# Optimization experiments

Hardware: AMD Instinct MI355X
Metric: run time of the kernel (lower is better)

Reference implementation:

```python
import jax, jax.numpy as jnp
import numpy as np

N = 50000
E = 800000
HEADS = 4
C = 64  # per-head channels
IN = 256
NEG_SLOPE = 0.2


def setup_inputs() -> dict:
    key = jax.random.key(0)
    k = jax.random.split(key, 6)
    x = jax.random.normal(k[0], (N, IN), dtype=jnp.float32)
    edge_index = jax.random.randint(k[1], (2, E), 0, N, dtype=jnp.int64)
    # Glorot-ish scale for weights
    W = jax.random.normal(k[2], (IN, HEADS * C), dtype=jnp.float32) * (1.0 / np.sqrt(IN))
    att_src = jax.random.normal(k[3], (HEADS, C), dtype=jnp.float32) * (1.0 / np.sqrt(C))
    att_dst = jax.random.normal(k[4], (HEADS, C), dtype=jnp.float32) * (1.0 / np.sqrt(C))
    bias = jax.random.normal(k[5], (HEADS * C,), dtype=jnp.float32) * 0.02
    return {"x": x, "edge_index": edge_index, "W": W, "att_src": att_src,
            "att_dst": att_dst, "bias": bias}


def _gat_forward(x, edge_index, W, att_src, att_dst, bias):
    n = x.shape[0]
    h = (x @ W).reshape(n, HEADS, C)  # [N, H, C]

    # add self loops (PyG default add_self_loops=True)
    loop = jnp.arange(n, dtype=edge_index.dtype)
    src = jnp.concatenate([edge_index[0], loop])  # [E+N]
    dst = jnp.concatenate([edge_index[1], loop])

    # per-node attention contributions  [N, H]
    a_src = jnp.einsum('nhc,hc->nh', h, att_src)
    a_dst = jnp.einsum('nhc,hc->nh', h, att_dst)

    # edge logits with leaky relu  [E+N, H]
    logits = a_src[src] + a_dst[dst]
    logits = jnp.where(logits >= 0, logits, NEG_SLOPE * logits)

    # segment softmax over destination neighborhoods
    seg_max = jax.ops.segment_max(logits, dst, num_segments=n)  # [N, H]
    seg_max = jnp.where(jnp.isfinite(seg_max), seg_max, 0.0)
    ex = jnp.exp(logits - seg_max[dst])
    denom = jax.ops.segment_sum(ex, dst, num_segments=n)  # [N, H]
    alpha = ex / (denom[dst] + 1e-16)  # [E+N, H]

    # weighted scatter-add of source messages
    msgs = alpha[:, :, None] * h[src]  # [E+N, H, C]
    out = jax.ops.segment_sum(msgs, dst, num_segments=n)  # [N, H, C]
    out = out.reshape(n, HEADS * C) + bias
    return jax.nn.relu(out)


def reference(x, edge_index, W, att_src, att_dst, bias):
    return _gat_forward(x, edge_index, W, att_src, att_dst, bias)
```

## Files before the change

### kernel.cpp

```cpp
#include <hip/hip_runtime.h>
#include <hip/hip_bf16.h>
#include <math.h>

#define NEG 0.2f
#define BSH 5
#define EPB 2048

typedef __attribute__((ext_vector_type(4))) float f4;
typedef __attribute__((ext_vector_type(8))) short s8;
typedef __attribute__((ext_vector_type(2))) __fp16 h2;

__device__ __forceinline__ short f2bf(float f) {
    unsigned u = __float_as_uint(f);
    u += 0x7fff + ((u >> 16) & 1);
    return (short)(u >> 16);
}
__device__ __forceinline__ unsigned pk2(float a, float b) {
    union { __hip_bfloat162 h; unsigned u; } c;
    c.h = __float22bfloat162_rn(make_float2(a, b));
    return c.u;
}
__device__ __forceinline__ unsigned pkh(float a, float b) {
    union { h2 h; unsigned u; } c;
    c.h = __builtin_amdgcn_cvt_pkrtz(a, b);
    return c.u;
}
__device__ __forceinline__ void fma8(float* acc, float w, uint4 v) {
    union { uint4 u; __fp16 h[8]; } c; c.u = v;
#pragma unroll
    for (int k = 0; k < 8; ++k) acc[k] = fmaf(w, (float)c.h[k], acc[k]);
}

__global__ __launch_bounds__(256) void prep_count(
    const float* __restrict__ W, short* __restrict__ Wt, int* __restrict__ off,
    const int* __restrict__ ei, int* __restrict__ hist2d,
    int E, int N, int NBUCK, int NB, int Etot)
{
    const int blk = blockIdx.x, t = threadIdx.x;
    if (blk < 256) {
        int id = blk * 256 + t;
        int n = id >> 8, k = id & 255;
        Wt[id] = f2bf(W[k * 256 + n]);
        if (id == 0) off[N] = Etot;
        return;
    }
    extern __shared__ int lh[];
    const int cblk = blk - 256;
    for (int b = t; b < NBUCK; b += 256) lh[b] = 0;
    __syncthreads();
    const int e0 = cblk * EPB;
    if (e0 + EPB <= E) {
#pragma unroll
        for (int i = 0; i < EPB / 1024; ++i) {
            int e = e0 + i * 1024 + t * 4;
            int4 d = *(const int4*)(ei + E + e);
            atomicAdd(&lh[d.x >> BSH], 1);
            atomicAdd(&lh[d.y >> BSH], 1);
            atomicAdd(&lh[d.z >> BSH], 1);
            atomicAdd(&lh[d.w >> BSH], 1);
        }
    } else {
        for (int i = 0; i < EPB / 256; ++i) {
            int e = e0 + i * 256 + t;
            if (e < Etot) {
                int dte = (e < E) ? ei[E + e] : (e - E);
                atomicAdd(&lh[dte >> BSH], 1);
            }
        }
    }
    __syncthreads();
    for (int b = t; b < NBUCK; b += 256) hist2d[b * NB + cblk] = lh[b];
}

__global__ __launch_bounds__(512) void gemm_attn(
    const float* __restrict__ x, const short* __restrict__ Wt,
    const float* __restrict__ att_src, const float* __restrict__ att_dst,
    short* __restrict__ hb, float* __restrict__ a_src_n,
    float* __restrict__ a_dst_n, int M)
{
    __shared__ __align__(16) short xs[2][128][32];
    const int t = threadIdx.x;
    const int lane = t & 63, wv = t >> 6;
    const int wr = wv >> 2;
    const int hd = wv & 3;
    const int quad = lane >> 4, l15 = lane & 15;
    const int n0 = blockIdx.x * 128;

    const int row = t >> 2, kq = t & 3;
    const bool okr = (n0 + row) < M;
    const float* xp = x + (size_t)(n0 + row) * 256 + kq * 8;

    const short* wbase = Wt + (size_t)(hd * 64 + l15) * 256 + quad * 8;

    f4 acc[4][4];
#pragma unroll
    for (int i = 0; i < 4; ++i)
#pragma unroll
        for (int j = 0; j < 4; ++j) acc[i][j] = (f4)(0.f);

    float4 v0 = {}, v1 = {};
    if (okr) { const float4* p = (const float4*)xp; v0 = p[0]; v1 = p[1]; }

    int buf = 0;
#pragma unroll
    for (int ks = 0; ks < 8; ++ks) {
        uint4 u = { pk2(v0.x, v0.y), pk2(v0.z, v0.w), pk2(v1.x, v1.y), pk2(v1.z, v1.w) };
        *(uint4*)&xs[buf][row][kq * 8] = u;
        __syncthreads();

        if (ks < 7 && okr) {
            const float4* p = (const float4*)(xp + (ks + 1) * 32);
            v0 = p[0]; v1 = p[1];
        }

        s8 af[4], bf[4];
#pragma unroll
        for (int i = 0; i < 4; ++i)
            af[i] = *(const s8*)(wbase + (size_t)(i * 16) * 256 + ks * 32);
#pragma unroll
        for (int j = 0; j < 4; ++j)
            bf[j] = *(const s8*)&xs[buf][wr * 64 + j * 16 + l15][quad * 8];
#pragma unroll
        for (int i = 0; i < 4; ++i)
#pragma unroll
            for (int j = 0; j < 4; ++j)
                acc[i][j] = __builtin_amdgcn_mfma_f32_16x16x32_bf16(af[i], bf[j], acc[i][j], 0, 0, 0);
        buf ^= 1;
    }

    float asv[4][4], adv[4][4];
#pragma unroll
    for (int i = 0; i < 4; ++i)
#pragma unroll
        for (int rr = 0; rr < 4; ++rr) {
            asv[i][rr] = att_src[hd * 64 + i * 16 + quad * 4 + rr];
            adv[i][rr] = att_dst[hd * 64 + i * 16 + quad * 4 + rr];
        }

#pragma unroll
    for (int j = 0; j < 4; ++j) {
        const int node = n0 + wr * 64 + j * 16 + l15;
        const bool ok = node < M;
        float ps = 0.f, pd = 0.f;
#pragma unroll
        for (int i = 0; i < 4; ++i)
#pragma unroll
            for (int rr = 0; rr < 4; ++rr) {
                float v = acc[i][j][rr];
                ps = fmaf(v, asv[i][rr], ps);
                pd = fmaf(v, adv[i][rr], pd);
            }
        ps += __shfl_xor(ps, 16); ps += __shfl_xor(ps, 32);
        pd += __shfl_xor(pd, 16); pd += __shfl_xor(pd, 32);
        if (ok && quad == 0) {
            a_src_n[node * 4 + hd] = ps;
            a_dst_n[node * 4 + hd] = pd;
        }
        if (ok) {
#pragma unroll
            for (int i = 0; i < 4; ++i) {
                uint2 pk = make_uint2(pkh(acc[i][j][0], acc[i][j][1]),
                                      pkh(acc[i][j][2], acc[i][j][3]));
                *(uint2*)&hb[(size_t)node * 256 + hd * 64 + i * 16 + quad * 4] = pk;
            }
        }
    }
}

__global__ __launch_bounds__(1024) void scan1(const int* __restrict__ src,
                                              int* __restrict__ dst,
                                              int* __restrict__ bsum, int Ntot)
{
    __shared__ int wsum[16], wexc[16];
    const int t = threadIdx.x, lane = t & 63, w = t >> 6;
    const int idx = blockIdx.x * 1024 + t;
    int v = (idx < Ntot) ? src[idx] : 0;
    int val = v;
#pragma unroll
    for (int o = 1; o < 64; o <<= 1) {
        int u = __shfl_up(val, o);
        if (lane >= o) val += u;
    }
    if (lane == 63) wsum[w] = val;
    __syncthreads();
    if (t < 16) {
        int s = wsum[t];
#pragma unroll
        for (int o = 1; o < 16; o <<= 1) {
            int u = __shfl_up(s, o, 16);
            if (t >= o) s += u;
        }
        wexc[t] = s - wsum[t];
        if (t == 15) bsum[blockIdx.x] = s;
    }
    __syncthreads();
    if (idx < Ntot) dst[idx] = wexc[w] + val - v;
}

__global__ __launch_bounds__(1024) void scan2v(const int* __restrict__ bsum,
                                               int* __restrict__ bexc, int nb)
{
    __shared__ int wsum[16], wexc[16];
    const int t = threadIdx.x, lane = t & 63, w = t >> 6;
    int v = (t < nb) ? bsum[t] : 0;
    int val = v;
#pragma unroll
    for (int o = 1; o < 64; o <<= 1) {
        int u = __shfl_up(val, o);
        if (lane >= o) val += u;
    }
    if (lane == 63) wsum[w] = val;
    __syncthreads();
    if (t < 16) {
        int s = wsum[t];
#pragma unroll
        for (int o = 1; o < 16; o <<= 1) {
            int u = __shfl_up(s, o, 16);
            if (t >= o) s += u;
        }
        wexc[t] = s - wsum[t];
    }
    __syncthreads();
    if (t < nb) bexc[t] = wexc[w] + val - v;
}

__global__ __launch_bounds__(256) void scatter2(const int* __restrict__ ei,
                                                const int* __restrict__ scanned,
                                                const int* __restrict__ bexc,
                                                unsigned* __restrict__ bucketed,
                                                int E, int N, int NBUCK, int NB)
{
    extern __shared__ int lcur[];
    const int t = threadIdx.x, blk = blockIdx.x;
    for (int b = t; b < NBUCK; b += 256) {
        int idx = b * NB + blk;
        lcur[b] = scanned[idx] + bexc[idx >> 10];
    }
    __syncthreads();
    const int e0 = blk * EPB, Etot = E + N;
    if (e0 + EPB <= E) {
#pragma unroll
        for (int i = 0; i < EPB / 1024; ++i) {
            int e = e0 + i * 1024 + t * 4;
            int4 s4 = *(const int4*)(ei + e);
            int4 d4 = *(const int4*)(ei + E + e);
            int p0 = atomicAdd(&lcur[d4.x >> BSH], 1);
            bucketed[p0] = (unsigned)s4.x | ((unsigned)(d4.x & 31) << 20);
            int p1 = atomicAdd(&lcur[d4.y >> BSH], 1);
            bucketed[p1] = (unsigned)s4.y | ((unsigned)(d4.y & 31) << 20);
            int p2 = atomicAdd(&lcur[d4.z >> BSH], 1);
            bucketed[p2] = (unsigned)s4.z | ((unsigned)(d4.z & 31) << 20);
            int p3 = atomicAdd(&lcur[d4.w >> BSH], 1);
            bucketed[p3] = (unsigned)s4.w | ((unsigned)(d4.w & 31) << 20);
        }
    } else {
        for (int i = 0; i < EPB / 256; ++i) {
            int e = e0 + i * 256 + t;
            if (e < Etot) {
                int src, dte;
                if (e < E) { src = ei[e]; dte = ei[E + e]; }
                else       { src = e - E; dte = src; }
                int pos = atomicAdd(&lcur[dte >> BSH], 1);
                bucketed[pos] = (unsigned)src | ((unsigned)(dte & 31) << 20);
            }
        }
    }
}

__global__ __launch_bounds__(256) void csr_build(
    const unsigned* __restrict__ bucketed, const int* __restrict__ scanned,
    const int* __restrict__ bexc, int* __restrict__ off, int* __restrict__ csr,
    int N, int NB, int NBUCK, int Etot)
{
    __shared__ unsigned est[2048];
    __shared__ int ldeg4[4][32], lcur4[4][32], loff[32];
    const int t = threadIdx.x, wv = t >> 6, b = blockIdx.x;

    const int i0 = b * NB;
    const int gbase = scanned[i0] + bexc[i0 >> 10];
    int gend;
    if (b + 1 == NBUCK) gend = Etot;
    else { int i1 = (b + 1) * NB; gend = scanned[i1] + bexc[i1 >> 10]; }
    int cnt = gend - gbase;
    if (cnt > 2048) cnt = 2048;

    if (t < 128) ldeg4[t >> 5][t & 31] = 0;
    __syncthreads();
    for (int i = t; i < cnt; i += 256) {
        unsigned en = bucketed[gbase + i];
        est[i] = en;
        atomicAdd(&ldeg4[wv][en >> 20], 1);
    }
    __syncthreads();
    if (t < 32) {
        int d0 = ldeg4[0][t], d1 = ldeg4[1][t], d2 = ldeg4[2][t], d3 = ldeg4[3][t];
        int tot = d0 + d1 + d2 + d3;
        int val = tot;
#pragma unroll
        for (int o = 1; o < 32; o <<= 1) {
            int u = __shfl_up(val, o, 32);
            if (t >= o) val += u;
        }
        int excl = val - tot;
        loff[t] = excl;
        lcur4[0][t] = excl;
        lcur4[1][t] = excl + d0;
        lcur4[2][t] = excl + d0 + d1;
        lcur4[3][t] = excl + d0 + d1 + d2;
    }
    __syncthreads();
    for (int i = t; i < cnt; i += 256) {
        unsigned en = est[i];
        int pos = atomicAdd(&lcur4[wv][en >> 20], 1);
        csr[gbase + pos] = (int)(en & 0xFFFFF);
    }
    if (t < 32) {
        int n = (b << BSH) + t;
        if (n < N) off[n] = gbase + loff[t];
    }
}

__global__ __launch_bounds__(256) void aggregate(const short* __restrict__ hb,
                                                 const float* __restrict__ a_src_n,
                                                 const float* __restrict__ a_dst_n,
                                                 const int* __restrict__ off,
                                                 const int* __restrict__ csr,
                                                 const float* __restrict__ bias,
                                                 float* __restrict__ out, int N)
{
    __shared__ float lds_w[4][64][4];
    __shared__ int   lds_s[4][64];
    const int wv = threadIdx.x >> 6;
    const int lane = threadIdx.x & 63;
    const int half = lane >> 5, l31 = lane & 31;
    const int n = blockIdx.x * 4 + wv;
    if (n >= N) return;

    const int base = off[n];
    const int d = off[n + 1] - base;
    const float4 ad = *(const float4*)(a_dst_n + 4 * n);
    const int hl = l31 >> 3;

    float acc[8] = {0.f, 0.f, 0.f, 0.f, 0.f, 0.f, 0.f, 0.f};
    float4 sum = make_float4(0.f, 0.f, 0.f, 0.f);
    const uint4* hp = (const uint4*)hb;

    for (int c0 = 0; c0 < d; c0 += 64) {
        int j = c0 + lane;
        int s = 0;
        float4 w4 = make_float4(0.f, 0.f, 0.f, 0.f);
        if (j < d) {
            s = csr[base + j];
            float4 as = *(const float4*)(a_src_n + 4 * s);
            float lx = as.x + ad.x; lx = lx >= 0.f ? lx : NEG * lx;
            float ly = as.y + ad.y; ly = ly >= 0.f ? ly : NEG * ly;
            float lz = as.z + ad.z; lz = lz >= 0.f ? lz : NEG * lz;
            float lw = as.w + ad.w; lw = lw >= 0.f ? lw : NEG * lw;
            w4 = make_float4(__expf(lx), __expf(ly), __expf(lz), __expf(lw));
        }
        sum.x += w4.x; sum.y += w4.y; sum.z += w4.z; sum.w += w4.w;
        *(float4*)&lds_w[wv][lane][0] = w4;
        lds_s[wv][lane] = s;
        __builtin_amdgcn_wave_barrier();

        const int cl = (d - c0) < 64 ? (d - c0) : 64;
        int jj = 0;
        for (; jj + 8 <= cl; jj += 8) {
            int   s0 = lds_s[wv][jj + half];
            int   s1 = lds_s[wv][jj + 2 + half];
            int   s2 = lds_s[wv][jj + 4 + half];
            int   s3 = lds_s[wv][jj + 6 + half];
            float w0 = lds_w[wv][jj + half][hl];
            float w1 = lds_w[wv][jj + 2 + half][hl];
            float w2 = lds_w[wv][jj + 4 + half][hl];
            float w3 = lds_w[wv][jj + 6 + half][hl];
            uint4 v0 = hp[(size_t)s0 * 32 + l31];
            uint4 v1 = hp[(size_t)s1 * 32 + l31];
            uint4 v2 = hp[(size_t)s2 * 32 + l31];
            uint4 v3 = hp[(size_t)s3 * 32 + l31];
            fma8(acc, w0, v0);
            fma8(acc, w1, v1);
            fma8(acc, w2, v2);
            fma8(acc, w3, v3);
        }
        for (; jj < cl; jj += 2) {
            int   s0 = lds_s[wv][jj + half];
            float w0 = lds_w[wv][jj + half][hl];
            uint4 v0 = hp[(size_t)s0 * 32 + l31];
            fma8(acc, w0, v0);
        }
        __builtin_amdgcn_wave_barrier();
    }

#pragma unroll
    for (int k = 0; k < 8; ++k) acc[k] += __shfl_xor(acc[k], 32);

#pragma unroll
    for (int o = 32; o > 0; o >>= 1) {
        sum.x += __shfl_xor(sum.x, o);
        sum.y += __shfl_xor(sum.y, o);
        sum.z += __shfl_xor(sum.z, o);
        sum.w += __shfl_xor(sum.w, o);
    }
    float sh = (hl & 2) ? ((hl & 1) ? sum.w : sum.z) : ((hl & 1) ? sum.y : sum.x);
    float ih = 1.f / (sh + 1e-16f);

    if (half == 0) {
        const float4* bp = (const float4*)bias + l31 * 2;
        float4 b0 = bp[0], b1 = bp[1];
        float4 o0, o1;
        o0.x = fmaxf(fmaf(acc[0], ih, b0.x), 0.f);
        o0.y = fmaxf(fmaf(acc[1], ih, b0.y), 0.f);
        o0.z = fmaxf(fmaf(acc[2], ih, b0.z), 0.f);
        o0.w = fmaxf(fmaf(acc[3], ih, b0.w), 0.f);
        o1.x = fmaxf(fmaf(acc[4], ih, b1.x), 0.f);
        o1.y = fmaxf(fmaf(acc[5], ih, b1.y), 0.f);
        o1.z = fmaxf(fmaf(acc[6], ih, b1.z), 0.f);
        o1.w = fmaxf(fmaf(acc[7], ih, b1.w), 0.f);
        float4* op = (float4*)(out + (size_t)n * 256) + l31 * 2;
        op[0] = o0;
        op[1] = o1;
    }
}

extern "C" void kernel_launch(void* const* d_in, const int* in_sizes, int n_in,
                              void* d_out, int out_size, void* d_ws, size_t ws_size,
                              hipStream_t stream)
{
    const float* x       = (const float*)d_in[0];
    const int*   ei      = (const int*)d_in[1];
    const float* W       = (const float*)d_in[2];
    const float* att_src = (const float*)d_in[3];
    const float* att_dst = (const float*)d_in[4];
    const float* bias    = (const float*)d_in[5];
    float* out = (float*)d_out;

    const int N = in_sizes[0] / 256;
    const int E = in_sizes[1] / 2;
    const int Etot = E + N;
    const int NBUCK = (N + 31) >> BSH;
    const int NB = (Etot + EPB - 1) / EPB;
    const int Ntot = NBUCK * NB;
    const int nb1 = (Ntot + 1023) / 1024;

    char* p = (char*)d_ws;
    short*    hb      = (short*)p;    p += (size_t)N * 256 * sizeof(short);
    short*    Wt      = (short*)p;    p += 256 * 256 * sizeof(short);
    float*    a_src_n = (float*)p;    p += (size_t)N * 4 * sizeof(float);
    float*    a_dst_n = (float*)p;    p += (size_t)N * 4 * sizeof(float);
    int*      hist2d  = (int*)p;      p += (size_t)Ntot * sizeof(int);
    int*      scanned = (int*)p;      p += (size_t)Ntot * sizeof(int);
    int*      bsum    = (int*)p;      p += 1024 * sizeof(int);
    int*      bexc    = (int*)p;      p += 1024 * sizeof(int);
    int*      off     = (int*)p;      p += (size_t)(N + 1) * sizeof(int);
    unsigned* bucketed= (unsigned*)p; p += (size_t)Etot * sizeof(unsigned);
    int*      csr     = (int*)p;      p += (size_t)Etot * sizeof(int);

    prep_count<<<256 + NB, 256, NBUCK * sizeof(int), stream>>>(
        W, Wt, off, ei, hist2d, E, N, NBUCK, NB, Etot);
    gemm_attn<<<(N + 127) / 128, 512, 0, stream>>>(
        x, Wt, att_src, att_dst, hb, a_src_n, a_dst_n, N);
    scan1<<<nb1, 1024, 0, stream>>>(hist2d, scanned, bsum, Ntot);
    scan2v<<<1, 1024, 0, stream>>>(bsum, bexc, nb1);
    scatter2<<<NB, 256, NBUCK * sizeof(int), stream>>>(ei, scanned, bexc, bucketed,
                                                       E, N, NBUCK, NB);
    csr_build<<<NBUCK, 256, 0, stream>>>(bucketed, scanned, bexc, off, csr,
                                         N, NB, NBUCK, Etot);
    aggregate<<<(N + 3) / 4, 256, 0, stream>>>(hb, a_src_n, a_dst_n, off, csr,
                                               bias, out, N);
}
```

Measured before the change: 234.0 us.

## Process two nodes per wave with software-pipelined gather in aggregate

The aggregate kernel now gives each half-wave (32 lanes) its own destination node, so a wave handles two nodes and the grid is halved. Source indices are broadcast with shuffles instead of through LDS. The per-chunk gather is unrolled over 32 edges, keeping eight row loads in flight ahead of the FMAs. This removes the cross-half accumulator reduction and aims to hide gather latency, at the cost of more registers and divergence when the two nodes' degrees differ.

```diff
diff --git a/kernel.cpp b/kernel.cpp
--- a/kernel.cpp
+++ b/kernel.cpp
@@ -329,29 +329,46 @@
                                                  float* __restrict__ out, int N)
 {
     __shared__ float lds_w[4][64][4];
-    __shared__ int   lds_s[4][64];
-    const int wv = threadIdx.x >> 6;
-    const int lane = threadIdx.x & 63;
+    const int t = threadIdx.x, wv = t >> 6, lane = t & 63;
     const int half = lane >> 5, l31 = lane & 31;
-    const int n = blockIdx.x * 4 + wv;
-    if (n >= N) return;
-
-    const int base = off[n];
-    const int d = off[n + 1] - base;
-    const float4 ad = *(const float4*)(a_dst_n + 4 * n);
+    const int hsel = lane & 32;
+    const int n = blockIdx.x * 8 + wv * 2 + half;
+    const bool okn = n < N;
+    const int nc = okn ? n : (N - 1);
+
+    const int base = off[nc];
+    const int d = off[nc + 1] - base;
+    const float4 ad = *(const float4*)(a_dst_n + 4 * nc);
     const int hl = l31 >> 3;
+    const uint4* hp = (const uint4*)hb;
 
     float acc[8] = {0.f, 0.f, 0.f, 0.f, 0.f, 0.f, 0.f, 0.f};
     float4 sum = make_float4(0.f, 0.f, 0.f, 0.f);
-    const uint4* hp = (const uint4*)hb;
-
-    for (int c0 = 0; c0 < d; c0 += 64) {
-        int j = c0 + lane;
-        int s = 0;
+
+    int dm = d; { int o = __shfl_xor(d, 32); dm = dm > o ? dm : o; }
+    const int tc = (dm + 31) >> 5;
+
+    for (int c = 0; c < tc; ++c) {
+        const int c0 = c << 5;
+        const int j = c0 + l31;
+        const int jc = (j < d) ? j : (d - 1);
+        const int s_my = csr[base + jc];
+
+        const int cl = d - c0;
+        const int Sown = cl < 0 ? 0 : (cl > 32 ? 32 : cl);
+        int S = Sown; { int o = __shfl_xor(Sown, 32); S = S > o ? S : o; }
+
+        const float4 as = *(const float4*)(a_src_n + 4 * s_my);
+
+        uint4 va0 = {}, va1 = {}, va2 = {}, va3 = {};
+        uint4 vb0 = {}, vb1 = {}, vb2 = {}, vb3 = {};
+#define ISS(K, V) if ((K) < S) { int sk = __shfl(s_my, hsel | (K)); \
+                                 V = hp[(size_t)sk * 32 + l31]; }
+        ISS(0, va0) ISS(1, va1) ISS(2, va2) ISS(3, va3)
+        ISS(4, vb0) ISS(5, vb1) ISS(6, vb2) ISS(7, vb3)
+
         float4 w4 = make_float4(0.f, 0.f, 0.f, 0.f);
         if (j < d) {
-            s = csr[base + j];
-            float4 as = *(const float4*)(a_src_n + 4 * s);
             float lx = as.x + ad.x; lx = lx >= 0.f ? lx : NEG * lx;
             float ly = as.y + ad.y; ly = ly >= 0.f ? ly : NEG * ly;
             float lz = as.z + ad.z; lz = lz >= 0.f ? lz : NEG * lz;
@@ -360,43 +377,27 @@
         }
         sum.x += w4.x; sum.y += w4.y; sum.z += w4.z; sum.w += w4.w;
         *(float4*)&lds_w[wv][lane][0] = w4;
-        lds_s[wv][lane] = s;
         __builtin_amdgcn_wave_barrier();
 
-        const int cl = (d - c0) < 64 ? (d - c0) : 64;
-        int jj = 0;
-        for (; jj + 8 <= cl; jj += 8) {
-            int   s0 = lds_s[wv][jj + half];
-            int   s1 = lds_s[wv][jj + 2 + half];
-            int   s2 = lds_s[wv][jj + 4 + half];
-            int   s3 = lds_s[wv][jj + 6 + half];
-            float w0 = lds_w[wv][jj + half][hl];
-            float w1 = lds_w[wv][jj + 2 + half][hl];
-            float w2 = lds_w[wv][jj + 4 + half][hl];
-            float w3 = lds_w[wv][jj + 6 + half][hl];
-            uint4 v0 = hp[(size_t)s0 * 32 + l31];
-            uint4 v1 = hp[(size_t)s1 * 32 + l31];
-            uint4 v2 = hp[(size_t)s2 * 32 + l31];
-            uint4 v3 = hp[(size_t)s3 * 32 + l31];
-            fma8(acc, w0, v0);
-            fma8(acc, w1, v1);
-            fma8(acc, w2, v2);
-            fma8(acc, w3, v3);
-        }
-        for (; jj < cl; jj += 2) {
-            int   s0 = lds_s[wv][jj + half];
-            float w0 = lds_w[wv][jj + half][hl];
-            uint4 v0 = hp[(size_t)s0 * 32 + l31];
-            fma8(acc, w0, v0);
-        }
+#define CON(K, V) if ((K) < S) { float wk = lds_w[wv][hsel | (K)][hl]; \
+                                 fma8(acc, wk, V); }
+#define STP(K, V) CON(K, V) ISS((K) + 8, V)
+        STP(0, va0)  STP(1, va1)  STP(2, va2)  STP(3, va3)
+        STP(4, vb0)  STP(5, vb1)  STP(6, vb2)  STP(7, vb3)
+        STP(8, va0)  STP(9, va1)  STP(10, va2) STP(11, va3)
+        STP(12, vb0) STP(13, vb1) STP(14, vb2) STP(15, vb3)
+        STP(16, va0) STP(17, va1) STP(18, va2) STP(19, va3)
+        STP(20, vb0) STP(21, vb1) STP(22, vb2) STP(23, vb3)
+        CON(24, va0) CON(25, va1) CON(26, va2) CON(27, va3)
+        CON(28, vb0) CON(29, vb1) CON(30, vb2) CON(31, vb3)
+#undef STP
+#undef CON
+#undef ISS
         __builtin_amdgcn_wave_barrier();
     }
 
 #pragma unroll
-    for (int k = 0; k < 8; ++k) acc[k] += __shfl_xor(acc[k], 32);
-
-#pragma unroll
-    for (int o = 32; o > 0; o >>= 1) {
+    for (int o = 16; o > 0; o >>= 1) {
         sum.x += __shfl_xor(sum.x, o);
         sum.y += __shfl_xor(sum.y, o);
         sum.z += __shfl_xor(sum.z, o);
@@ -405,7 +406,7 @@
     float sh = (hl & 2) ? ((hl & 1) ? sum.w : sum.z) : ((hl & 1) ? sum.y : sum.x);
     float ih = 1.f / (sh + 1e-16f);
 
-    if (half == 0) {
+    if (okn) {
         const float4* bp = (const float4*)bias + l31 * 2;
         float4 b0 = bp[0], b1 = bp[1];
         float4 o0, o1;
@@ -466,6 +467,6 @@
                                                        E, N, NBUCK, NB);
     csr_build<<<NBUCK, 256, 0, stream>>>(bucketed, scanned, bexc, off, csr,
                                          N, NB, NBUCK, Etot);
-    aggregate<<<(N + 3) / 4, 256, 0, stream>>>(hb, a_src_n, a_dst_n, off, csr,
+    aggregate<<<(N + 7) / 8, 256, 0, stream>>>(hb, a_src_n, a_dst_n, off, csr,
                                                bias, out, N);
 }
```

New measurement: 246.2 us. 5.2% more time.
